# Performance work log

Hardware: AMD Instinct MI355X
Metric: run time of the kernel (lower is better)

## Reference

```python
import jax, jax.numpy as jnp
import numpy as np

N_INPUT = 64
HIDDEN = 32
N_OUTPUT = 24
N_BD_LAYERS = 4  # len(n_hidden) - 1 for n_hidden=[32]*5


def _filters():
    # 4 blocks of 8x8 ones on the diagonal -> 32x32 mask
    hid_filter = jnp.kron(jnp.eye(4, dtype=jnp.float32), jnp.ones((8, 8), jnp.float32))
    # 8 blocks of 4x3 ones -> 32x24 mask
    out_filter = jnp.kron(jnp.eye(8, dtype=jnp.float32), jnp.ones((4, 3), jnp.float32))
    return hid_filter, out_filter


def setup_inputs() -> dict:
    key = jax.random.key(0)
    k_x, k_in, k_h, k_out = jax.random.split(key, 4)
    B = 1048576
    x = jax.random.normal(k_x, (B, N_INPUT), dtype=jnp.float32)
    # torch initializes these weights with torch.rand (uniform [0,1))
    input_weight = jax.random.uniform(k_in, (N_INPUT, HIDDEN), dtype=jnp.float32)
    hidden_weights = jax.random.uniform(k_h, (N_BD_LAYERS, HIDDEN, HIDDEN), dtype=jnp.float32)
    output_weights = jax.random.uniform(k_out, (HIDDEN, N_OUTPUT), dtype=jnp.float32)
    return {
        "x": x,
        "input_weight": input_weight,
        "hidden_weights": hidden_weights,
        "output_weights": output_weights,
    }


def reference(x, input_weight, hidden_weights, output_weights):
    hid_filter, out_filter = _filters()
    # Fully-connected input layer + relu (dropout_p=0 / eval -> identity)
    h = jax.nn.relu(x @ input_weight)  # [B, 32]

    # Block-diagonal hidden layers: mask-multiplied dense matmul, relu
    def step(h, w):
        return jax.nn.relu(h @ (hid_filter * w)), None

    h, _ = jax.lax.scan(step, h, hidden_weights)
    # Block-diagonal output layer (no activation)
    out = h @ (out_filter * output_weights)  # [B, 24]
    return out
```

## Files before the change

### kernel.cpp

```cpp
#include <hip/hip_runtime.h>


typedef _Float16 f16;
typedef __attribute__((ext_vector_type(4))) _Float16 f16x4;
typedef __attribute__((ext_vector_type(8))) _Float16 f16x8;
typedef __attribute__((ext_vector_type(4))) float f32x4;

#define WS_WH  2048
#define WS_WO  6144
#define WS_TOT 7168

#define WAITV(N) asm volatile("s_waitcnt vmcnt(" #N ")" ::: "memory")

__global__ void repack_kernel(const float* __restrict__ Win,
                              const float* __restrict__ Wh,
                              const float* __restrict__ Wout,
                              f16* __restrict__ ws)
{
    int i = blockIdx.x * 256 + threadIdx.x;
    if (i >= WS_TOT) return;
    float val;
    if (i < WS_WH) {
        int fi = i >> 9, rest = i & 511;
        int l = rest >> 3, j = rest & 7;
        int h = fi >> 1, s = fi & 1;
        int g = l >> 4, m = l & 15;
        int k = 32 * s + 8 * g + j;
        val = Win[k * 32 + 16 * h + m];
    } else if (i < WS_WO) {
        int t2 = i - WS_WH;
        int fi = t2 >> 8, rest = t2 & 255;
        int l = rest >> 2, j = rest & 3;
        int t = fi >> 2, h = (fi >> 1) & 1, s = fi & 1;
        int g = l >> 4, m = l & 15;
        int k = 16 * s + 4 * g + j, col = 16 * h + m;
        val = ((k >> 3) == (col >> 3)) ? Wh[t * 1024 + k * 32 + col] : 0.f;
    } else {
        int t2 = i - WS_WO;
        int fi = t2 >> 8, rest = t2 & 255;
        int l = rest >> 2, j = rest & 3;
        int h = fi >> 1, s = fi & 1;
        int g = l >> 4, m = l & 15;
        int k = 16 * s + 4 * g + j, col = 16 * h + m;
        val = (col < 24 && (k >> 2) == (col / 3)) ? Wout[k * 24 + col] : 0.f;
    }
    ws[i] = (f16)val;
}

__global__ __launch_bounds__(256, 2)
void bd_mlp_kernel(const float* __restrict__ x,
                   const f16* __restrict__ ws,
                   const float* __restrict__ Win,
                   const float* __restrict__ Wh,
                   const float* __restrict__ Wout,
                   float* __restrict__ out,
                   int B)
{
    __shared__ __align__(16) float lds[4][2][2048];

    const int tid  = threadIdx.x;
    const int wid  = tid >> 6;
    const int lane = tid & 63;
    const int g    = lane >> 4;
    const int b    = lane & 15;

    const int wave_id = blockIdx.x * 4 + wid;
    const int nwaves  = gridDim.x * 4;
    const int ntiles  = B >> 5;

    f16x8 wina[2][2];
#pragma unroll
    for (int h = 0; h < 2; ++h)
#pragma unroll
        for (int s = 0; s < 2; ++s)
            wina[h][s] = __builtin_bit_cast(f16x8,
                *reinterpret_cast<const f32x4*>(
                    ws + (h * 2 + s) * 512 + lane * 8));

    f16x4 wha[4][2][2];
#pragma unroll
    for (int t = 0; t < 4; ++t)
#pragma unroll
        for (int h = 0; h < 2; ++h)
#pragma unroll
            for (int s = 0; s < 2; ++s)
                wha[t][h][s] = __builtin_bit_cast(f16x4,
                    *reinterpret_cast<const float2*>(
                        ws + WS_WH + (t * 4 + h * 2 + s) * 256 + lane * 4));

    f16x4 woa[2][2];
#pragma unroll
    for (int h = 0; h < 2; ++h)
#pragma unroll
        for (int s = 0; s < 2; ++s)
            woa[h][s] = __builtin_bit_cast(f16x4,
                *reinterpret_cast<const float2*>(
                    ws + WS_WO + (h * 2 + s) * 256 + lane * 4));

    const f32x4 zero = {0.f, 0.f, 0.f, 0.f};

    int nt = 0;
    if (wave_id < ntiles) nt = (ntiles - wave_id - 1) / nwaves + 1;

    auto STAGE = [&](int bufi, int tile) {
        float* tb = &lds[wid][bufi][0];
        const int rowbase = tile << 5;
#pragma unroll
        for (int j = 0; j < 8; ++j) {
            const int r  = 4 * j + (lane >> 4);
            const int gs = (lane & 15) ^ (r & 7);
            const float* src = x + (size_t)(rowbase + r) * 64 + gs * 4;
            __builtin_amdgcn_global_load_lds(
                (const __attribute__((address_space(1))) void*)src,
                (__attribute__((address_space(3))) void*)(tb + j * 256),
                16, 0, 0);
        }
    };

    if (nt > 0) {
        STAGE(0, wave_id);
        if (nt > 1) STAGE(1, wave_id + nwaves);

        for (int i = 0; i < nt; ++i) {
            if (i == 0)           { if (nt > 1) WAITV(8); else WAITV(0); }
            else if (i + 1 == nt) WAITV(4);
            else                  WAITV(12);
            __builtin_amdgcn_sched_barrier(0);

            const float* tb = &lds[wid][i & 1][0];
            const int rowbase = (wave_id + i * nwaves) << 5;

            f32x4 raw[2][2][2];
#pragma unroll
            for (int c = 0; c < 2; ++c)
#pragma unroll
                for (int s = 0; s < 2; ++s)
#pragma unroll
                    for (int hh = 0; hh < 2; ++hh)
                        raw[c][s][hh] = *reinterpret_cast<const f32x4*>(
                            tb + (16 * c + b) * 64 +
                            4 * ((2 * g + 8 * s + hh) ^ (b & 7)));
            asm volatile("s_waitcnt lgkmcnt(0)" ::: "memory");
            __builtin_amdgcn_sched_barrier(0);

            if (i + 2 < nt) STAGE(i & 1, wave_id + (i + 2) * nwaves);

#pragma unroll
            for (int c = 0; c < 2; ++c) {
                f16x8 bx[2];
#pragma unroll
                for (int s = 0; s < 2; ++s) {
                    f32x4 u0 = raw[c][s][0];
                    f32x4 u1 = raw[c][s][1];
                    f16x8 v;
                    v[0] = (f16)u0[0]; v[1] = (f16)u0[1];
                    v[2] = (f16)u0[2]; v[3] = (f16)u0[3];
                    v[4] = (f16)u1[0]; v[5] = (f16)u1[1];
                    v[6] = (f16)u1[2]; v[7] = (f16)u1[3];
                    bx[s] = v;
                }

                f32x4 t0 = __builtin_amdgcn_mfma_f32_16x16x32_f16(
                    wina[0][0], bx[0], zero, 0, 0, 0);
                t0 = __builtin_amdgcn_mfma_f32_16x16x32_f16(
                    wina[0][1], bx[1], t0, 0, 0, 0);
                f32x4 t1 = __builtin_amdgcn_mfma_f32_16x16x32_f16(
                    wina[1][0], bx[0], zero, 0, 0, 0);
                t1 = __builtin_amdgcn_mfma_f32_16x16x32_f16(
                    wina[1][1], bx[1], t1, 0, 0, 0);

                f16x4 hb0, hb1;
#pragma unroll
                for (int j = 0; j < 4; ++j) {
                    hb0[j] = (f16)fmaxf(t0[j], 0.f);
                    hb1[j] = (f16)fmaxf(t1[j], 0.f);
                }

#pragma unroll
                for (int t = 0; t < 4; ++t) {
                    f32x4 n0 = __builtin_amdgcn_mfma_f32_16x16x16f16(
                        wha[t][0][0], hb0, zero, 0, 0, 0);
                    n0 = __builtin_amdgcn_mfma_f32_16x16x16f16(
                        wha[t][0][1], hb1, n0, 0, 0, 0);
                    f32x4 n1 = __builtin_amdgcn_mfma_f32_16x16x16f16(
                        wha[t][1][0], hb0, zero, 0, 0, 0);
                    n1 = __builtin_amdgcn_mfma_f32_16x16x16f16(
                        wha[t][1][1], hb1, n1, 0, 0, 0);
#pragma unroll
                    for (int j = 0; j < 4; ++j) {
                        hb0[j] = (f16)fmaxf(n0[j], 0.f);
                        hb1[j] = (f16)fmaxf(n1[j], 0.f);
                    }
                }

                f32x4 o0 = __builtin_amdgcn_mfma_f32_16x16x16f16(
                    woa[0][0], hb0, zero, 0, 0, 0);
                o0 = __builtin_amdgcn_mfma_f32_16x16x16f16(
                    woa[0][1], hb1, o0, 0, 0, 0);
                f32x4 o1 = __builtin_amdgcn_mfma_f32_16x16x16f16(
                    woa[1][0], hb0, zero, 0, 0, 0);
                o1 = __builtin_amdgcn_mfma_f32_16x16x16f16(
                    woa[1][1], hb1, o1, 0, 0, 0);

                float* op = out + (size_t)(rowbase + 16 * c + b) * 24;
                __builtin_nontemporal_store(
                    o0, reinterpret_cast<f32x4*>(op + 4 * g));
                if (g < 2) {
                    __builtin_nontemporal_store(
                        o1, reinterpret_cast<f32x4*>(op + 16 + 4 * g));
                }
            }
        }
    }

    if (blockIdx.x == 0 && wid == 0) {
        for (int row = (ntiles << 5) + lane; row < B; row += 64) {
            float h[32];
#pragma unroll
            for (int j = 0; j < 32; ++j) h[j] = 0.f;
            const float* __restrict__ xr = x + (size_t)row * 64;
            for (int k = 0; k < 64; ++k) {
                float xv = xr[k];
#pragma unroll
                for (int j = 0; j < 32; ++j)
                    h[j] = fmaf(xv, Win[k * 32 + j], h[j]);
            }
#pragma unroll
            for (int j = 0; j < 32; ++j) h[j] = fmaxf(h[j], 0.f);
            for (int t = 0; t < 4; ++t) {
                float hn[32];
                for (int j = 0; j < 32; ++j) {
                    float acc = 0.f;
                    int blk = j >> 3;
                    for (int k = 0; k < 8; ++k)
                        acc = fmaf(h[blk * 8 + k],
                                   Wh[t * 1024 + (blk * 8 + k) * 32 + j], acc);
                    hn[j] = fmaxf(acc, 0.f);
                }
                for (int j = 0; j < 32; ++j) h[j] = hn[j];
            }
            for (int cth = 0; cth < 24; ++cth) {
                int i8 = cth / 3;
                float acc = 0.f;
                for (int s = 0; s < 4; ++s)
                    acc = fmaf(h[4 * i8 + s], Wout[(4 * i8 + s) * 24 + cth], acc);
                out[(size_t)row * 24 + cth] = acc;
            }
        }
    }
}

extern "C" void kernel_launch(void* const* d_in, const int* in_sizes, int n_in,
                              void* d_out, int out_size, void* d_ws, size_t ws_size,
                              hipStream_t stream)
{
    const float* x    = (const float*)d_in[0];
    const float* Win  = (const float*)d_in[1];
    const float* Wh   = (const float*)d_in[2];
    const float* Wout = (const float*)d_in[3];
    float* out        = (float*)d_out;
    f16* ws           = (f16*)d_ws;

    int B = in_sizes[0] / 64;

    repack_kernel<<<(WS_TOT + 255) / 256, 256, 0, stream>>>(Win, Wh, Wout, ws);

    bd_mlp_kernel<<<1024, 256, 0, stream>>>(x, ws, Win, Wh, Wout, out, B);
}
```

Before: 67.31 us.

## Fold weight repacking into main kernel and halve grid size

Removes the separate repack kernel launch. Each wave now gathers and converts its MFMA weight fragments straight from the fp32 weight arrays, applying the block-diagonal masks inline. This drops one kernel launch and its dependency. The cost is that every wave does scattered scalar loads at startup. The grid also shrinks from 1024 to 512 blocks, so each wave handles more tiles and the per-wave weight setup is amortised over more work.

```diff
diff --git a/kernel.cpp b/kernel.cpp
--- a/kernel.cpp
+++ b/kernel.cpp
@@ -6,50 +6,10 @@
 typedef __attribute__((ext_vector_type(8))) _Float16 f16x8;
 typedef __attribute__((ext_vector_type(4))) float f32x4;
 
-#define WS_WH  2048
-#define WS_WO  6144
-#define WS_TOT 7168
-
 #define WAITV(N) asm volatile("s_waitcnt vmcnt(" #N ")" ::: "memory")
-
-__global__ void repack_kernel(const float* __restrict__ Win,
-                              const float* __restrict__ Wh,
-                              const float* __restrict__ Wout,
-                              f16* __restrict__ ws)
-{
-    int i = blockIdx.x * 256 + threadIdx.x;
-    if (i >= WS_TOT) return;
-    float val;
-    if (i < WS_WH) {
-        int fi = i >> 9, rest = i & 511;
-        int l = rest >> 3, j = rest & 7;
-        int h = fi >> 1, s = fi & 1;
-        int g = l >> 4, m = l & 15;
-        int k = 32 * s + 8 * g + j;
-        val = Win[k * 32 + 16 * h + m];
-    } else if (i < WS_WO) {
-        int t2 = i - WS_WH;
-        int fi = t2 >> 8, rest = t2 & 255;
-        int l = rest >> 2, j = rest & 3;
-        int t = fi >> 2, h = (fi >> 1) & 1, s = fi & 1;
-        int g = l >> 4, m = l & 15;
-        int k = 16 * s + 4 * g + j, col = 16 * h + m;
-        val = ((k >> 3) == (col >> 3)) ? Wh[t * 1024 + k * 32 + col] : 0.f;
-    } else {
-        int t2 = i - WS_WO;
-        int fi = t2 >> 8, rest = t2 & 255;
-        int l = rest >> 2, j = rest & 3;
-        int h = fi >> 1, s = fi & 1;
-        int g = l >> 4, m = l & 15;
-        int k = 16 * s + 4 * g + j, col = 16 * h + m;
-        val = (col < 24 && (k >> 2) == (col / 3)) ? Wout[k * 24 + col] : 0.f;
-    }
-    ws[i] = (f16)val;
-}
 
 __global__ __launch_bounds__(256, 2)
 void bd_mlp_kernel(const float* __restrict__ x,
-                   const f16* __restrict__ ws,
                    const float* __restrict__ Win,
                    const float* __restrict__ Wh,
                    const float* __restrict__ Wout,
@@ -72,10 +32,13 @@
 #pragma unroll
     for (int h = 0; h < 2; ++h)
 #pragma unroll
-        for (int s = 0; s < 2; ++s)
-            wina[h][s] = __builtin_bit_cast(f16x8,
-                *reinterpret_cast<const f32x4*>(
-                    ws + (h * 2 + s) * 512 + lane * 8));
+        for (int s = 0; s < 2; ++s) {
+            f16x8 v;
+#pragma unroll
+            for (int j = 0; j < 8; ++j)
+                v[j] = (f16)Win[(32 * s + 8 * g + j) * 32 + 16 * h + b];
+            wina[h][s] = v;
+        }
 
     f16x4 wha[4][2][2];
 #pragma unroll
@@ -83,19 +46,33 @@
 #pragma unroll
         for (int h = 0; h < 2; ++h)
 #pragma unroll
-            for (int s = 0; s < 2; ++s)
-                wha[t][h][s] = __builtin_bit_cast(f16x4,
-                    *reinterpret_cast<const float2*>(
-                        ws + WS_WH + (t * 4 + h * 2 + s) * 256 + lane * 4));
+            for (int s = 0; s < 2; ++s) {
+                const int col = 16 * h + b;
+                f16x4 v;
+#pragma unroll
+                for (int j = 0; j < 4; ++j) {
+                    const int k = 16 * s + 4 * g + j;
+                    v[j] = ((k >> 3) == (col >> 3))
+                             ? (f16)Wh[t * 1024 + k * 32 + col] : (f16)0.f;
+                }
+                wha[t][h][s] = v;
+            }
 
     f16x4 woa[2][2];
 #pragma unroll
     for (int h = 0; h < 2; ++h)
 #pragma unroll
-        for (int s = 0; s < 2; ++s)
-            woa[h][s] = __builtin_bit_cast(f16x4,
-                *reinterpret_cast<const float2*>(
-                    ws + WS_WO + (h * 2 + s) * 256 + lane * 4));
+        for (int s = 0; s < 2; ++s) {
+            const int col = 16 * h + b;
+            f16x4 v;
+#pragma unroll
+            for (int j = 0; j < 4; ++j) {
+                const int k = 16 * s + 4 * g + j;
+                v[j] = (col < 24 && (k >> 2) == (col / 3))
+                         ? (f16)Wout[k * 24 + col] : (f16)0.f;
+            }
+            woa[h][s] = v;
+        }
 
     const f32x4 zero = {0.f, 0.f, 0.f, 0.f};
 
@@ -259,11 +236,7 @@
     const float* Wh   = (const float*)d_in[2];
     const float* Wout = (const float*)d_in[3];
     float* out        = (float*)d_out;
-    f16* ws           = (f16*)d_ws;
 
     int B = in_sizes[0] / 64;
-
-    repack_kernel<<<(WS_TOT + 255) / 256, 256, 0, stream>>>(Win, Wh, Wout, ws);
-
-    bd_mlp_kernel<<<1024, 256, 0, stream>>>(x, ws, Win, Wh, Wout, out, B);
+    bd_mlp_kernel<<<512, 256, 0, stream>>>(x, Win, Wh, Wout, out, B);
 }
```

After: 72.33 us. 7.5% more time.
